# Kernel tuning notes

Measured on AMD Instinct MI355X. Metric: run time of the kernel, lower is better.

## Reference

```python
import jax, jax.numpy as jnp
import numpy as np

NHEADS = 16
HEAD_DIM = 64
HIDDEN = 1024
QKV = NHEADS * HEAD_DIM  # 1024
SCALING = HEAD_DIM ** -0.5


def setup_inputs() -> dict:
    key = jax.random.key(0)
    k1, k2, k3, k4, k5 = jax.random.split(key, 5)
    B, S = 2, 2048
    hidden_states = jax.random.normal(k1, (B, S, HIDDEN), dtype=jnp.float32)
    # nn.Linear weights: stored [out, in]; kaiming-uniform-ish init scale
    w_qkv = jax.random.normal(k2, (3 * QKV, HIDDEN), dtype=jnp.float32) * (HIDDEN ** -0.5)
    b_qkv = jax.random.normal(k3, (3 * QKV,), dtype=jnp.float32) * 0.01
    w_o = jax.random.normal(k4, (HIDDEN, QKV), dtype=jnp.float32) * (QKV ** -0.5)
    b_o = jax.random.normal(k5, (HIDDEN,), dtype=jnp.float32) * 0.01
    return {"hidden_states": hidden_states, "w_qkv": w_qkv, "b_qkv": b_qkv,
            "w_o": w_o, "b_o": b_o}


def reference(hidden_states, w_qkv, b_qkv, w_o, b_o):
    B, S, _ = hidden_states.shape
    # qkv projection: x @ W^T + b  (torch nn.Linear convention)
    qkv = jnp.einsum('bsh,oh->bso', hidden_states, w_qkv) + b_qkv  # [B,S,3*QKV]
    xq, xk, xv = jnp.split(qkv, 3, axis=-1)
    # [B,S,H,D] -> [B,H,S,D]
    q = xq.reshape(B, S, NHEADS, HEAD_DIM).transpose(0, 2, 1, 3)
    k = xk.reshape(B, S, NHEADS, HEAD_DIM).transpose(0, 2, 1, 3)
    v = xv.reshape(B, S, NHEADS, HEAD_DIM).transpose(0, 2, 1, 3)
    scores = jnp.einsum('bhqd,bhkd->bhqk', q, k) * SCALING
    # dropout is identity in eval mode; mask is None in this config
    probs = jax.nn.softmax(scores.astype(jnp.float32), axis=-1).astype(q.dtype)
    out = jnp.einsum('bhqk,bhkd->bhqd', probs, v)  # [B,H,S,D]
    out = out.transpose(0, 2, 1, 3).reshape(B, S, QKV)
    return jnp.einsum('bsq,oq->bso', out, w_o) + b_o
```

## Files before the change

### kernel.cpp

```cpp
#include <hip/hip_runtime.h>

#define SEQ     2048
#define MROWS   4096
#define HID     1024
#define QKV3    3072
#define NH      16
#define HD      64
#define QSCALE  0.18033688f

typedef unsigned short u16;
typedef unsigned int   u32;
typedef __attribute__((ext_vector_type(8)))  short  bf16x8;
typedef __attribute__((ext_vector_type(4)))  float  floatx4;

__device__ __forceinline__ u16 f2bf(float f) {
    u32 u = __builtin_bit_cast(u32, f);
    u += 0x7fffu + ((u >> 16) & 1u);
    return (u16)(u >> 16);
}

#if __has_builtin(__builtin_amdgcn_exp2f)
__device__ __forceinline__ float fast_exp2(float x) { return __builtin_amdgcn_exp2f(x); }
#else
__device__ __forceinline__ float fast_exp2(float x) { return exp2f(x); }
#endif

#if __has_builtin(__builtin_amdgcn_cvt_pk_bf16_f32)
__device__ __forceinline__ u32 pack_bf(float a, float b) {
    auto r = __builtin_amdgcn_cvt_pk_bf16_f32(a, b);
    return __builtin_bit_cast(u32, r);
}
#else
__device__ __forceinline__ u32 pack_bf(float a, float b) {
    u32 ua = __builtin_bit_cast(u32, a) + 0x8000u;
    u32 ub = __builtin_bit_cast(u32, b) + 0x8000u;
    return __builtin_amdgcn_perm(ub, ua, 0x07060302u);
}
#endif

__device__ __forceinline__ void async_cp16(const void* g, void* l) {
    __builtin_amdgcn_global_load_lds(
        (const __attribute__((address_space(1))) unsigned int*)g,
        (__attribute__((address_space(3))) unsigned int*)l, 16, 0, 0);
}

#define N4_X   (MROWS * HID / 4)
#define N4_WQ  (QKV3 * HID / 4)
#define N4_WO  (HID * HID / 4)
__global__ void cvt_all(const float* __restrict__ x, const float* __restrict__ wq,
                        const float* __restrict__ wo, u16* __restrict__ xb,
                        u16* __restrict__ wqb, u16* __restrict__ wob) {
    int i = blockIdx.x * blockDim.x + threadIdx.x;
    const float* src; u16* dst; int k;
    if (i < N4_X)                { src = x;  dst = xb;  k = i; }
    else if (i < N4_X + N4_WQ)   { src = wq; dst = wqb; k = i - N4_X; }
    else                         { src = wo; dst = wob; k = i - N4_X - N4_WQ; }
    float4 v = ((const float4*)src)[k];
    uint2 o = {pack_bf(v.x, v.y), pack_bf(v.z, v.w)};
    ((uint2*)dst)[k] = o;
}

template <int MODE, int NT>
__global__ __launch_bounds__(256)
void gemm_bf16_nt(const u16* __restrict__ A, const u16* __restrict__ B,
                  const float* __restrict__ bias, float* __restrict__ Cout,
                  int M, int N, int K,
                  u16* __restrict__ q_ws, u16* __restrict__ k_ws,
                  u16* __restrict__ vt_ws) {
    constexpr int WN = NT / 2;
    constexpr int NJ = WN / 16;
    __shared__ u16 As[2][128 * 32];
    __shared__ u16 Bs[2][NT * 32];
    const int t  = (int)threadIdx.x;
    const int w  = t >> 6, l = t & 63;
    const int wr = w >> 1, wc = w & 1;
    const int m0 = (int)blockIdx.y * 128, n0 = (int)blockIdx.x * NT;
    const int lrow = l >> 2;
    const int lseg = ((l & 3) ^ ((l >> 3) & 3)) * 8;
    const int fm = l & 15, fq = l >> 4;
    const int fseg = (fq ^ ((fm >> 1) & 3)) * 8;

    auto stage = [&](int k0, int bb) {
#pragma unroll
        for (int rep = 0; rep < 2; ++rep) {
            const int chunk = w + rep * 4;
            const int row   = chunk * 16 + lrow;
            async_cp16(A + (size_t)(m0 + row) * K + k0 + lseg, &As[bb][chunk * 512]);
            if (NT == 128 || rep == 0)
                async_cp16(B + (size_t)(n0 + row) * K + k0 + lseg, &Bs[bb][chunk * 512]);
        }
    };

    floatx4 acc[4][NJ];
#pragma unroll
    for (int i = 0; i < 4; ++i)
#pragma unroll
        for (int j = 0; j < NJ; ++j) acc[i][j] = (floatx4)(0.f);

    const int T = K >> 5;
    stage(0, 0);
    for (int tt = 0; tt < T; ++tt) {
        const int cur = tt & 1;
        __syncthreads();
        if (tt + 1 < T) stage((tt + 1) << 5, cur ^ 1);
        bf16x8 af[4], bf[NJ];
#pragma unroll
        for (int i = 0; i < 4; ++i)
            af[i] = *(const bf16x8*)&As[cur][(wr * 64 + i * 16 + fm) * 32 + fseg];
#pragma unroll
        for (int j = 0; j < NJ; ++j)
            bf[j] = *(const bf16x8*)&Bs[cur][(wc * WN + j * 16 + fm) * 32 + fseg];
#pragma unroll
        for (int i = 0; i < 4; ++i)
#pragma unroll
            for (int j = 0; j < NJ; ++j)
                acc[i][j] = __builtin_amdgcn_mfma_f32_16x16x32_bf16(
                    af[i], bf[j], acc[i][j], 0, 0, 0);
    }

#pragma unroll
    for (int j = 0; j < NJ; ++j) {
        const int col = n0 + wc * WN + j * 16 + fm;
        const float bv = bias[col];
        const int region = col >> 10;
        const int hh = (col >> 6) & 15, d = col & 63;
#pragma unroll
        for (int i = 0; i < 4; ++i) {
            const int row0 = m0 + wr * 64 + i * 16 + fq * 4;
            if (MODE == 0) {
#pragma unroll
                for (int r = 0; r < 4; ++r)
                    Cout[(size_t)(row0 + r) * N + col] = acc[i][j][r] + bv;
            } else if (region < 2) {
                u16* __restrict__ dst = (region == 0) ? q_ws : k_ws;
                const float sc = (region == 0) ? QSCALE : 1.0f;
#pragma unroll
                for (int r = 0; r < 4; ++r) {
                    const int row = row0 + r;
                    const int b = row >> 11, s = row & 2047;
                    dst[((size_t)(b * NH + hh) * SEQ + s) * HD + d] =
                        f2bf((acc[i][j][r] + bv) * sc);
                }
            } else {
                const int b = row0 >> 11, s0 = row0 & 2047;
                uint2 o = {pack_bf(acc[i][j][0] + bv, acc[i][j][1] + bv),
                           pack_bf(acc[i][j][2] + bv, acc[i][j][3] + bv)};
                *(uint2*)&vt_ws[((size_t)(b * NH + hh) * HD + d) * SEQ + s0] = o;
            }
        }
    }
}

__global__ __launch_bounds__(256, 2)
void attn_mfma(const u16* __restrict__ qw, const u16* __restrict__ kw,
               const u16* __restrict__ vtw, u16* __restrict__ attn) {
    __shared__ u16 Ks [2][64 * 64];
    __shared__ u16 Vts[2][64 * 64];
    __shared__ u16 Ps[4][32 * 72];

    const int bh   = (int)blockIdx.x;
    const int qblk = (int)blockIdx.y * 128;
    const int t = (int)threadIdx.x;
    const int w = t >> 6, l = t & 63;
    const int fm = l & 15, fq = l >> 4;
    const int srow = l >> 3, sseg = l & 7;
    const size_t headSD = (size_t)bh * SEQ * HD;
    const size_t headDS = (size_t)bh * HD * SEQ;

    auto stage = [&](int kt, int bb) {
#pragma unroll
        for (int rep = 0; rep < 2; ++rep) {
            const int chunk = w * 2 + rep;
            async_cp16(kw + headSD + (size_t)(kt * 64 + chunk * 8 + srow) * HD
                           + ((sseg ^ srow) * 8), &Ks[bb][chunk * 512]);
            async_cp16(vtw + headDS + (size_t)(chunk * 8 + srow) * SEQ + kt * 64
                           + ((sseg ^ srow) * 8), &Vts[bb][chunk * 512]);
        }
    };

    bf16x8 qa[2][2];
#pragma unroll
    for (int qs = 0; qs < 2; ++qs)
#pragma unroll
        for (int kc = 0; kc < 2; ++kc)
            qa[qs][kc] = *(const bf16x8*)(qw + headSD
                + (size_t)(qblk + w * 32 + qs * 16 + fm) * HD + kc * 32 + fq * 8);

    floatx4 oacc[2][4];
#pragma unroll
    for (int qs = 0; qs < 2; ++qs)
#pragma unroll
        for (int dt = 0; dt < 4; ++dt) oacc[qs][dt] = (floatx4)(0.f);
    float psum[2] = {0.f, 0.f};

    stage(0, 0);
    for (int kt = 0; kt < SEQ / 64; ++kt) {
        const int cur = kt & 1;
        __syncthreads();
        if (kt + 1 < SEQ / 64) stage(kt + 1, cur ^ 1);

        floatx4 sacc[2][4];
#pragma unroll
        for (int qs = 0; qs < 2; ++qs)
#pragma unroll
            for (int j = 0; j < 4; ++j) sacc[qs][j] = (floatx4)(0.f);
        __builtin_amdgcn_s_setprio(1);
#pragma unroll
        for (int j = 0; j < 4; ++j) {
#pragma unroll
            for (int kc = 0; kc < 2; ++kc) {
                const int seg = (4 * kc + fq) ^ (fm & 7);
                bf16x8 ka = *(const bf16x8*)&Ks[cur][(j * 16 + fm) * 64 + seg * 8];
                sacc[0][j] = __builtin_amdgcn_mfma_f32_16x16x32_bf16(ka, qa[0][kc], sacc[0][j], 0, 0, 0);
                sacc[1][j] = __builtin_amdgcn_mfma_f32_16x16x32_bf16(ka, qa[1][kc], sacc[1][j], 0, 0, 0);
            }
        }
        __builtin_amdgcn_s_setprio(0);

#pragma unroll
        for (int qs = 0; qs < 2; ++qs) {
#pragma unroll
            for (int j = 0; j < 4; ++j) {
                const float p0 = fast_exp2(sacc[qs][j][0]);
                const float p1 = fast_exp2(sacc[qs][j][1]);
                const float p2 = fast_exp2(sacc[qs][j][2]);
                const float p3 = fast_exp2(sacc[qs][j][3]);
                psum[qs] += (p0 + p1) + (p2 + p3);
                uint2 pk = {pack_bf(p0, p1), pack_bf(p2, p3)};
                *(uint2*)&Ps[w][(qs * 16 + fm) * 72 + j * 16 + fq * 4] = pk;
            }
        }

        __builtin_amdgcn_s_setprio(1);
#pragma unroll
        for (int kc = 0; kc < 2; ++kc) {
            bf16x8 pb0 = *(const bf16x8*)&Ps[w][(fm) * 72 + kc * 32 + fq * 8];
            bf16x8 pb1 = *(const bf16x8*)&Ps[w][(16 + fm) * 72 + kc * 32 + fq * 8];
#pragma unroll
            for (int dt = 0; dt < 4; ++dt) {
                const int seg = (4 * kc + fq) ^ (fm & 7);
                bf16x8 va = *(const bf16x8*)&Vts[cur][(dt * 16 + fm) * 64 + seg * 8];
                oacc[0][dt] = __builtin_amdgcn_mfma_f32_16x16x32_bf16(
                    va, pb0, oacc[0][dt], 0, 0, 0);
                oacc[1][dt] = __builtin_amdgcn_mfma_f32_16x16x32_bf16(
                    va, pb1, oacc[1][dt], 0, 0, 0);
            }
        }
        __builtin_amdgcn_s_setprio(0);
    }

    const int b = bh >> 4, h = bh & 15;
#pragma unroll
    for (int qs = 0; qs < 2; ++qs) {
        float ps = psum[qs];
        ps += __shfl_xor(ps, 16);
        ps += __shfl_xor(ps, 32);
        const float inv = 1.0f / ps;
        u16* __restrict__ orow =
            attn + (size_t)(b * SEQ + qblk + w * 32 + qs * 16 + fm) * HID + h * HD;
#pragma unroll
        for (int dt = 0; dt < 4; ++dt) {
            uint2 o = {pack_bf(oacc[qs][dt][0] * inv, oacc[qs][dt][1] * inv),
                       pack_bf(oacc[qs][dt][2] * inv, oacc[qs][dt][3] * inv)};
            *(uint2*)&orow[dt * 16 + fq * 4] = o;
        }
    }
}

extern "C" void kernel_launch(void* const* d_in, const int* in_sizes, int n_in,
                              void* d_out, int out_size, void* d_ws, size_t ws_size,
                              hipStream_t stream) {
    const float* x     = (const float*)d_in[0];
    const float* w_qkv = (const float*)d_in[1];
    const float* b_qkv = (const float*)d_in[2];
    const float* w_o   = (const float*)d_in[3];
    const float* b_o   = (const float*)d_in[4];
    float* outp = (float*)d_out;

    u16* xb    = (u16*)d_ws;
    u16* wqkvb = xb    + (size_t)MROWS * HID;
    u16* wob   = wqkvb + (size_t)QKV3 * HID;
    u16* q_ws  = wob   + (size_t)HID * HID;
    u16* k_ws  = q_ws  + (size_t)MROWS * HID;
    u16* vt_ws = k_ws  + (size_t)MROWS * HID;
    u16* attnb = vt_ws + (size_t)MROWS * HID;

    const int blk = 256;
    cvt_all<<<(N4_X + N4_WQ + N4_WO) / blk, blk, 0, stream>>>(
        x, w_qkv, w_o, xb, wqkvb, wob);

    gemm_bf16_nt<1, 128><<<dim3(QKV3 / 128, MROWS / 128), blk, 0, stream>>>(
        xb, wqkvb, b_qkv, nullptr, MROWS, QKV3, HID, q_ws, k_ws, vt_ws);

    attn_mfma<<<dim3(NH * 2, SEQ / 128), 256, 0, stream>>>(q_ws, k_ws, vt_ws, attnb);

    gemm_bf16_nt<0, 64><<<dim3(HID / 64, MROWS / 128), blk, 0, stream>>>(
        attnb, wob, b_o, outp, MROWS, HID, HID, nullptr, nullptr, nullptr);
}
```

Baseline: 184.7 us.

## Use 32x32x16 MFMA in attention and keep P in registers via permlane swap

The attention inner loop switches from 16x16x32 MFMA tiles to 32x32x16 tiles, so each wave handles its 32 query rows in one tile. The softmax probabilities are packed to bf16 and rearranged across lanes with v_permlane32_swap, which lets them feed the PV MFMA directly instead of going through an LDS round trip (the per-wave Ps buffer is removed). This is meant to cut LDS traffic and instruction count, and the larger MFMA shape gives each K/V LDS read more reuse. The cost is larger accumulator register footprint and reliance on exact lane layouts for correctness.

```diff
diff --git a/kernel.cpp b/kernel.cpp
--- a/kernel.cpp
+++ b/kernel.cpp
@@ -12,6 +12,8 @@
 typedef unsigned int   u32;
 typedef __attribute__((ext_vector_type(8)))  short  bf16x8;
 typedef __attribute__((ext_vector_type(4)))  float  floatx4;
+typedef __attribute__((ext_vector_type(16))) float  floatx16;
+typedef __attribute__((ext_vector_type(4)))  unsigned int u32x4;
 
 __device__ __forceinline__ u16 f2bf(float f) {
     u32 u = __builtin_bit_cast(u32, f);
@@ -37,6 +39,16 @@
     return __builtin_amdgcn_perm(ub, ua, 0x07060302u);
 }
 #endif
+
+__device__ __forceinline__ void plane_swap(u32 &x, u32 &y) {
+#if __has_builtin(__builtin_amdgcn_permlane32_swap)
+    typedef __attribute__((ext_vector_type(2))) unsigned int u32x2;
+    u32x2 r = __builtin_amdgcn_permlane32_swap(x, y, false, false);
+    x = r[0]; y = r[1];
+#else
+    asm volatile("v_permlane32_swap_b32 %0, %1" : "+v"(x), "+v"(y));
+#endif
+}
 
 __device__ __forceinline__ void async_cp16(const void* g, void* l) {
     __builtin_amdgcn_global_load_lds(
@@ -156,13 +168,12 @@
                const u16* __restrict__ vtw, u16* __restrict__ attn) {
     __shared__ u16 Ks [2][64 * 64];
     __shared__ u16 Vts[2][64 * 64];
-    __shared__ u16 Ps[4][32 * 72];
 
     const int bh   = (int)blockIdx.x;
     const int qblk = (int)blockIdx.y * 128;
     const int t = (int)threadIdx.x;
     const int w = t >> 6, l = t & 63;
-    const int fm = l & 15, fq = l >> 4;
+    const int ql = l & 31, h = l >> 5;
     const int srow = l >> 3, sseg = l & 7;
     const size_t headSD = (size_t)bh * SEQ * HD;
     const size_t headDS = (size_t)bh * HD * SEQ;
@@ -178,20 +189,16 @@
         }
     };
 
-    bf16x8 qa[2][2];
-#pragma unroll
-    for (int qs = 0; qs < 2; ++qs)
-#pragma unroll
-        for (int kc = 0; kc < 2; ++kc)
-            qa[qs][kc] = *(const bf16x8*)(qw + headSD
-                + (size_t)(qblk + w * 32 + qs * 16 + fm) * HD + kc * 32 + fq * 8);
-
-    floatx4 oacc[2][4];
-#pragma unroll
-    for (int qs = 0; qs < 2; ++qs)
-#pragma unroll
-        for (int dt = 0; dt < 4; ++dt) oacc[qs][dt] = (floatx4)(0.f);
-    float psum[2] = {0.f, 0.f};
+    bf16x8 qa[4];
+#pragma unroll
+    for (int ks = 0; ks < 4; ++ks)
+        qa[ks] = *(const bf16x8*)(qw + headSD
+            + (size_t)(qblk + w * 32 + ql) * HD + ks * 16 + h * 8);
+
+    floatx16 oacc[2];
+#pragma unroll
+    for (int dt = 0; dt < 2; ++dt) oacc[dt] = (floatx16)(0.f);
+    float psum = 0.f;
 
     stage(0, 0);
     for (int kt = 0; kt < SEQ / 64; ++kt) {
@@ -199,70 +206,65 @@
         __syncthreads();
         if (kt + 1 < SEQ / 64) stage(kt + 1, cur ^ 1);
 
-        floatx4 sacc[2][4];
-#pragma unroll
-        for (int qs = 0; qs < 2; ++qs)
-#pragma unroll
-            for (int j = 0; j < 4; ++j) sacc[qs][j] = (floatx4)(0.f);
+        floatx16 sacc[2];
+        sacc[0] = (floatx16)(0.f); sacc[1] = (floatx16)(0.f);
         __builtin_amdgcn_s_setprio(1);
 #pragma unroll
-        for (int j = 0; j < 4; ++j) {
-#pragma unroll
-            for (int kc = 0; kc < 2; ++kc) {
-                const int seg = (4 * kc + fq) ^ (fm & 7);
-                bf16x8 ka = *(const bf16x8*)&Ks[cur][(j * 16 + fm) * 64 + seg * 8];
-                sacc[0][j] = __builtin_amdgcn_mfma_f32_16x16x32_bf16(ka, qa[0][kc], sacc[0][j], 0, 0, 0);
-                sacc[1][j] = __builtin_amdgcn_mfma_f32_16x16x32_bf16(ka, qa[1][kc], sacc[1][j], 0, 0, 0);
+        for (int ks = 0; ks < 4; ++ks) {
+            const int seg = (ks * 2 + h) ^ (ql & 7);
+#pragma unroll
+            for (int t2 = 0; t2 < 2; ++t2) {
+                bf16x8 ka = *(const bf16x8*)&Ks[cur][(t2 * 32 + ql) * 64 + seg * 8];
+                sacc[t2] = __builtin_amdgcn_mfma_f32_32x32x16_bf16(
+                    ka, qa[ks], sacc[t2], 0, 0, 0);
             }
         }
         __builtin_amdgcn_s_setprio(0);
 
 #pragma unroll
-        for (int qs = 0; qs < 2; ++qs) {
-#pragma unroll
-            for (int j = 0; j < 4; ++j) {
-                const float p0 = fast_exp2(sacc[qs][j][0]);
-                const float p1 = fast_exp2(sacc[qs][j][1]);
-                const float p2 = fast_exp2(sacc[qs][j][2]);
-                const float p3 = fast_exp2(sacc[qs][j][3]);
-                psum[qs] += (p0 + p1) + (p2 + p3);
-                uint2 pk = {pack_bf(p0, p1), pack_bf(p2, p3)};
-                *(uint2*)&Ps[w][(qs * 16 + fm) * 72 + j * 16 + fq * 4] = pk;
+        for (int t2 = 0; t2 < 2; ++t2) {
+            u32 aw[8];
+#pragma unroll
+            for (int i = 0; i < 8; ++i) {
+                const float p0 = fast_exp2(sacc[t2][2 * i]);
+                const float p1 = fast_exp2(sacc[t2][2 * i + 1]);
+                psum += p0 + p1;
+                aw[i] = pack_bf(p0, p1);
             }
-        }
-
-        __builtin_amdgcn_s_setprio(1);
-#pragma unroll
-        for (int kc = 0; kc < 2; ++kc) {
-            bf16x8 pb0 = *(const bf16x8*)&Ps[w][(fm) * 72 + kc * 32 + fq * 8];
-            bf16x8 pb1 = *(const bf16x8*)&Ps[w][(16 + fm) * 72 + kc * 32 + fq * 8];
-#pragma unroll
-            for (int dt = 0; dt < 4; ++dt) {
-                const int seg = (4 * kc + fq) ^ (fm & 7);
-                bf16x8 va = *(const bf16x8*)&Vts[cur][(dt * 16 + fm) * 64 + seg * 8];
-                oacc[0][dt] = __builtin_amdgcn_mfma_f32_16x16x32_bf16(
-                    va, pb0, oacc[0][dt], 0, 0, 0);
-                oacc[1][dt] = __builtin_amdgcn_mfma_f32_16x16x32_bf16(
-                    va, pb1, oacc[1][dt], 0, 0, 0);
+            plane_swap(aw[0], aw[2]); plane_swap(aw[1], aw[3]);
+            plane_swap(aw[4], aw[6]); plane_swap(aw[5], aw[7]);
+
+            __builtin_amdgcn_s_setprio(1);
+#pragma unroll
+            for (int ks2 = 0; ks2 < 2; ++ks2) {
+                u32x4 pw = {aw[4 * ks2 + 0], aw[4 * ks2 + 1],
+                            aw[4 * ks2 + 2], aw[4 * ks2 + 3]};
+                bf16x8 pb = __builtin_bit_cast(bf16x8, pw);
+                const int seg = (t2 * 4 + ks2 * 2 + h) ^ (ql & 7);
+#pragma unroll
+                for (int dt = 0; dt < 2; ++dt) {
+                    bf16x8 va = *(const bf16x8*)&Vts[cur][(dt * 32 + ql) * 64 + seg * 8];
+                    oacc[dt] = __builtin_amdgcn_mfma_f32_32x32x16_bf16(
+                        va, pb, oacc[dt], 0, 0, 0);
+                }
             }
-        }
-        __builtin_amdgcn_s_setprio(0);
+            __builtin_amdgcn_s_setprio(0);
+        }
     }
 
-    const int b = bh >> 4, h = bh & 15;
-#pragma unroll
-    for (int qs = 0; qs < 2; ++qs) {
-        float ps = psum[qs];
-        ps += __shfl_xor(ps, 16);
-        ps += __shfl_xor(ps, 32);
-        const float inv = 1.0f / ps;
-        u16* __restrict__ orow =
-            attn + (size_t)(b * SEQ + qblk + w * 32 + qs * 16 + fm) * HID + h * HD;
-#pragma unroll
-        for (int dt = 0; dt < 4; ++dt) {
-            uint2 o = {pack_bf(oacc[qs][dt][0] * inv, oacc[qs][dt][1] * inv),
-                       pack_bf(oacc[qs][dt][2] * inv, oacc[qs][dt][3] * inv)};
-            *(uint2*)&orow[dt * 16 + fq * 4] = o;
+    psum += __shfl_xor(psum, 32);
+    const float inv = 1.0f / psum;
+
+    const int b = bh >> 4, head = bh & 15;
+    u16* __restrict__ orow =
+        attn + (size_t)(b * SEQ + qblk + w * 32 + ql) * HID + head * HD;
+#pragma unroll
+    for (int dt = 0; dt < 2; ++dt) {
+#pragma unroll
+        for (int g = 0; g < 4; ++g) {
+            uint2 o = {pack_bf(oacc[dt][g * 4 + 0] * inv, oacc[dt][g * 4 + 1] * inv),
+                       pack_bf(oacc[dt][g * 4 + 2] * inv, oacc[dt][g * 4 + 3] * inv)};
+            *(uint2*)&orow[dt * 32 + g * 8 + h * 4] = o;
         }
     }
 }
```

New measurement: 187.4 us. Within noise of the previous version (+1.5%).
